# Kernel optimization log

Measured on AMD Instinct MI355X. Metric: run time of the kernel, lower is better.

The kernel has to match this reference:

```python
import jax, jax.numpy as jnp
import numpy as np

NUM_USERS = 100000
NUM_ITEMS = 50000
NUM_EDGES = 1000000
EMB_DIM = 64


def setup_inputs() -> dict:
    key = jax.random.key(0)
    k1, k2, k3, k4, k5, k6 = jax.random.split(key, 6)
    return {
        "user_emb": jax.random.normal(k1, (NUM_USERS, EMB_DIM), dtype=jnp.float32),
        "item_emb": jax.random.normal(k2, (NUM_ITEMS, EMB_DIM), dtype=jnp.float32),
        "u_sw": jax.random.uniform(k3, (NUM_USERS, 1), dtype=jnp.float32),
        "i_sw": jax.random.uniform(k4, (NUM_ITEMS, 1), dtype=jnp.float32),
        "edge_src_user": jax.random.randint(k5, (NUM_EDGES,), 0, NUM_USERS, dtype=jnp.int32),
        "edge_dst_item": jax.random.randint(k6, (NUM_EDGES,), 0, NUM_ITEMS, dtype=jnp.int32),
    }


def _segment_mean(feat_src, src_idx, dst_idx, num_dst, inv_deg):
    # gather source node features onto edges, sum-reduce at destinations, divide by degree
    s = jax.ops.segment_sum(feat_src[src_idx], dst_idx, num_segments=num_dst)
    return s * inv_deg


def reference(user_emb, item_emb, u_sw, i_sw, edge_src_user, edge_dst_item):
    ones = jnp.ones((edge_src_user.shape[0],), dtype=user_emb.dtype)
    deg_i = jax.ops.segment_sum(ones, edge_dst_item, num_segments=NUM_ITEMS)
    deg_u = jax.ops.segment_sum(ones, edge_src_user, num_segments=NUM_USERS)
    # DGL mean gives 0 for zero-degree nodes
    inv_deg_i = jnp.where(deg_i > 0, 1.0 / jnp.maximum(deg_i, 1.0), 0.0)[:, None]
    inv_deg_u = jnp.where(deg_u > 0, 1.0 / jnp.maximum(deg_u, 1.0), 0.0)[:, None]

    def one_round(u, i):
        # 'like': user -> item mean aggregation; 'rev_like': item -> user
        new_i = _segment_mean(u, edge_src_user, edge_dst_item, NUM_ITEMS, inv_deg_i)
        new_u = _segment_mean(i, edge_dst_item, edge_src_user, NUM_USERS, inv_deg_u)
        return new_u + u * u_sw, new_i + i * i_sw

    u, i = one_round(user_emb, item_emb)
    u, i = one_round(u, i)
    return (u, i)
```

## Files before the change

kernel.cpp:

```cpp
#include <hip/hip_runtime.h>
#include <hip/hip_fp16.h>

#define NU 100000
#define NI 50000
#define NE 1000000
#define D  64
#define NBI 196
#define NBU 391
#define NB_TOT (NBI + NBU)
#define CHUNK 2048
#define PART_K (CHUNK / 256)

__device__ __forceinline__ unsigned short f2h(float f) {
    return __half_as_ushort(__float2half(f));
}
__device__ __forceinline__ float h2f(unsigned short h) {
    return __half2float(__ushort_as_half(h));
}

__global__ void k_bhist_cvt(const int* __restrict__ esrc, const int* __restrict__ edst,
                            int* __restrict__ bcnt,
                            const float* __restrict__ ue, const float* __restrict__ ie,
                            unsigned short* __restrict__ u0h, unsigned short* __restrict__ i0h) {
    __shared__ int h[NB_TOT];
    for (int b = threadIdx.x; b < NB_TOT; b += blockDim.x) h[b] = 0;
    __syncthreads();
    int gt = blockIdx.x * blockDim.x + threadIdx.x;
    int gs = gridDim.x * blockDim.x;
    for (int e = gt; e < NE; e += gs) {
        atomicAdd(&h[edst[e] >> 8], 1);
        atomicAdd(&h[NBI + (esrc[e] >> 8)], 1);
    }
    const float4* uf = (const float4*)ue;
    ushort4* uh = (ushort4*)u0h;
    for (int i = gt; i < NU * (D / 4); i += gs) {
        float4 v = uf[i];
        ushort4 o; o.x = f2h(v.x); o.y = f2h(v.y); o.z = f2h(v.z); o.w = f2h(v.w);
        uh[i] = o;
    }
    const float4* if4 = (const float4*)ie;
    ushort4* ih = (ushort4*)i0h;
    for (int i = gt; i < NI * (D / 4); i += gs) {
        float4 v = if4[i];
        ushort4 o; o.x = f2h(v.x); o.y = f2h(v.y); o.z = f2h(v.z); o.w = f2h(v.w);
        ih[i] = o;
    }
    __syncthreads();
    for (int b = threadIdx.x; b < NB_TOT; b += blockDim.x) {
        int v = h[b];
        if (v) atomicAdd(&bcnt[b], v);
    }
}

__global__ void k_bscan_both(const int* __restrict__ bcnt,
                             int* __restrict__ bbase_i, int* __restrict__ gcur_i,
                             int* __restrict__ bbase_u, int* __restrict__ gcur_u) {
    __shared__ int s[512];
    int tid = threadIdx.x;
    const int* in = (blockIdx.x == 0) ? bcnt : bcnt + NBI;
    int nb        = (blockIdx.x == 0) ? NBI : NBU;
    int* bbase    = (blockIdx.x == 0) ? bbase_i : bbase_u;
    int* gcur     = (blockIdx.x == 0) ? gcur_i : gcur_u;
    int v = (tid < nb) ? in[tid] : 0;
    s[tid] = v;
    __syncthreads();
    for (int o = 1; o < 512; o <<= 1) {
        int t = (tid >= o) ? s[tid - o] : 0;
        __syncthreads();
        s[tid] += t;
        __syncthreads();
    }
    if (tid < nb) { int ex = s[tid] - v; bbase[tid] = ex; gcur[tid] = ex; }
    if (tid == 0) bbase[nb] = NE;
}

__global__ void k_part_both(const int* __restrict__ esrc, const int* __restrict__ edst,
                            int* __restrict__ gcur_i, int* __restrict__ gcur_u,
                            unsigned int* __restrict__ rec_i, unsigned int* __restrict__ rec_u) {
    __shared__ int cnt_i[NBI], gb_i[NBI], cnt_u[NBU], gb_u[NBU];
    int tid = threadIdx.x;
    for (int b = tid; b < NBI; b += 256) cnt_i[b] = 0;
    for (int b = tid; b < NBU; b += 256) cnt_u[b] = 0;
    __syncthreads();
    int base = blockIdx.x * CHUNK;
    int dd[PART_K], uu[PART_K], ki[PART_K], ku[PART_K];
#pragma unroll
    for (int k = 0; k < PART_K; k++) {
        int j = base + tid + k * 256;
        dd[k] = -1;
        if (j < NE) {
            dd[k] = edst[j]; uu[k] = esrc[j];
            ki[k] = atomicAdd(&cnt_i[dd[k] >> 8], 1);
            ku[k] = atomicAdd(&cnt_u[uu[k] >> 8], 1);
        }
    }
    __syncthreads();
    for (int b = tid; b < NBI; b += 256) { int v = cnt_i[b]; if (v) gb_i[b] = atomicAdd(&gcur_i[b], v); }
    for (int b = tid; b < NBU; b += 256) { int v = cnt_u[b]; if (v) gb_u[b] = atomicAdd(&gcur_u[b], v); }
    __syncthreads();
#pragma unroll
    for (int k = 0; k < PART_K; k++) {
        if (dd[k] >= 0) {
            rec_i[gb_i[dd[k] >> 8] + ki[k]] = ((unsigned int)(dd[k] & 255) << 17) | (unsigned int)uu[k];
            rec_u[gb_u[uu[k] >> 8] + ku[k]] = ((unsigned int)(uu[k] & 255) << 17) | (unsigned int)dd[k];
        }
    }
}

__global__ void k_local_both(const unsigned int* __restrict__ rec_i, const unsigned int* __restrict__ rec_u,
                             const int* __restrict__ bbase_i, const int* __restrict__ bbase_u,
                             int* __restrict__ rp_i, int* __restrict__ rp_u,
                             int* __restrict__ col_i, int* __restrict__ col_u) {
    __shared__ int cnt[256];
    __shared__ int off[256];
    int tid = threadIdx.x;
    int t = blockIdx.x;
    bool item = t < NBI;
    int b = item ? t : t - NBI;
    const unsigned int* rec = item ? rec_i : rec_u;
    const int* bb = item ? bbase_i : bbase_u;
    int* rp  = item ? rp_i : rp_u;
    int* col = item ? col_i : col_u;
    int nn   = item ? NI : NU;
    int beg = bb[b], end = bb[b + 1];
    cnt[tid] = 0;
    __syncthreads();
    for (int j = beg + tid; j < end; j += 256)
        atomicAdd(&cnt[rec[j] >> 17], 1);
    __syncthreads();
    int v = cnt[tid];
    off[tid] = v;
    __syncthreads();
    for (int o = 1; o < 256; o <<= 1) {
        int tv = (tid >= o) ? off[tid - o] : 0;
        __syncthreads();
        off[tid] += tv;
        __syncthreads();
    }
    int ex = off[tid] - v;
    int node = b * 256 + tid;
    if (node <= nn) rp[node] = beg + ex;
    cnt[tid] = ex;
    __syncthreads();
    for (int j = beg + tid; j < end; j += 256) {
        unsigned int r = rec[j];
        int p = atomicAdd(&cnt[r >> 17], 1);
        col[beg + p] = (int)(r & 0x1FFFF);
    }
}

template<bool WF, bool WH>
__device__ __forceinline__ void agg_h(const unsigned short* __restrict__ feat,
        const unsigned short* selfh, const float* __restrict__ sw,
        const int* __restrict__ rp, const int* __restrict__ cols,
        float* __restrict__ outf, unsigned short* outh,
        int n, int li, int lb) {
    int beg = rp[n], end = rp[n + 1];
    float swv = sw[n];
    ushort4 s4 = *(const ushort4*)(selfh + (size_t)n * D + li * 4);
    float ax = 0.f, ay = 0.f, az = 0.f, aw = 0.f;
    for (int j0 = beg; j0 < end; j0 += 16) {
        int cv = (j0 + li < end) ? cols[j0 + li] : 0;
        int nj = end - j0;
        ushort4 h[16];
#pragma unroll
        for (int j = 0; j < 16; j++) {
            int c = __shfl(cv, lb + j, 64);
            h[j] = *(const ushort4*)(feat + (size_t)c * D + li * 4);
        }
#pragma unroll
        for (int j = 0; j < 16; j++) {
            float w = (j < nj) ? 1.0f : 0.0f;
            ax = fmaf(w, h2f(h[j].x), ax);
            ay = fmaf(w, h2f(h[j].y), ay);
            az = fmaf(w, h2f(h[j].z), az);
            aw = fmaf(w, h2f(h[j].w), aw);
        }
    }
    int dgr = end - beg;
    float inv = (dgr > 0) ? (1.0f / (float)dgr) : 0.0f;
    float rx = ax * inv + h2f(s4.x) * swv;
    float ry = ay * inv + h2f(s4.y) * swv;
    float rz = az * inv + h2f(s4.z) * swv;
    float rw = aw * inv + h2f(s4.w) * swv;
    if (WH) {
        ushort4 o; o.x = f2h(rx); o.y = f2h(ry); o.z = f2h(rz); o.w = f2h(rw);
        *(ushort4*)(outh + (size_t)n * D + li * 4) = o;
    }
    if (WF) {
        float4 o; o.x = rx; o.y = ry; o.z = rz; o.w = rw;
        *(float4*)(outf + (size_t)n * D + li * 4) = o;
    }
}

__global__ __launch_bounds__(256) void k_agg_r1(
        const unsigned short* __restrict__ u0h, const unsigned short* __restrict__ i0h,
        const float* __restrict__ u_sw, const float* __restrict__ i_sw,
        const int* __restrict__ rp_i, const int* __restrict__ rp_u,
        const int* __restrict__ col_i, const int* __restrict__ col_u,
        unsigned short* __restrict__ i1h, unsigned short* __restrict__ u1h) {
    int g  = (blockIdx.x * blockDim.x + threadIdx.x) >> 4;
    int li = threadIdx.x & 15;
    int lb = threadIdx.x & 48;
    if (g < NI)
        agg_h<false, true>(u0h, i0h, i_sw, rp_i, col_i, nullptr, i1h, g, li, lb);
    else
        agg_h<false, true>(i0h, u0h, u_sw, rp_u, col_u, nullptr, u1h, g - NI, li, lb);
}

__global__ __launch_bounds__(256) void k_agg_r1i(
        const unsigned short* __restrict__ u0h, const unsigned short* __restrict__ i0h,
        const float* __restrict__ i_sw,
        const int* __restrict__ rp_i, const int* __restrict__ col_i,
        unsigned short* __restrict__ i1h) {
    int g  = (blockIdx.x * blockDim.x + threadIdx.x) >> 4;
    if (g >= NI) return;
    agg_h<false, true>(u0h, i0h, i_sw, rp_i, col_i, nullptr, i1h, g, threadIdx.x & 15, threadIdx.x & 48);
}
__global__ __launch_bounds__(256) void k_agg_r1u(
        const unsigned short* __restrict__ i0h, const unsigned short* u0h,
        const float* __restrict__ u_sw,
        const int* __restrict__ rp_u, const int* __restrict__ col_u,
        unsigned short* u1h) {
    int g  = (blockIdx.x * blockDim.x + threadIdx.x) >> 4;
    if (g >= NU) return;
    agg_h<false, true>(i0h, u0h, u_sw, rp_u, col_u, nullptr, u1h, g, threadIdx.x & 15, threadIdx.x & 48);
}

__global__ __launch_bounds__(256) void k_agg_r2(
        const unsigned short* __restrict__ u1h, const unsigned short* __restrict__ i1h,
        const float* __restrict__ u_sw, const float* __restrict__ i_sw,
        const int* __restrict__ rp_i, const int* __restrict__ rp_u,
        const int* __restrict__ col_i, const int* __restrict__ col_u,
        float* __restrict__ out_i, float* __restrict__ out_u) {
    int g  = (blockIdx.x * blockDim.x + threadIdx.x) >> 4;
    int li = threadIdx.x & 15;
    int lb = threadIdx.x & 48;
    if (g < NI)
        agg_h<true, false>(u1h, i1h, i_sw, rp_i, col_i, out_i, nullptr, g, li, lb);
    else
        agg_h<true, false>(i1h, u1h, u_sw, rp_u, col_u, out_u, nullptr, g - NI, li, lb);
}

extern "C" void kernel_launch(void* const* d_in, const int* in_sizes, int n_in,
                              void* d_out, int out_size, void* d_ws, size_t ws_size,
                              hipStream_t stream) {
    const float* user_emb = (const float*)d_in[0];
    const float* item_emb = (const float*)d_in[1];
    const float* u_sw     = (const float*)d_in[2];
    const float* i_sw     = (const float*)d_in[3];
    const int*   esrc     = (const int*)d_in[4];
    const int*   edst     = (const int*)d_in[5];

    float* out_u = (float*)d_out;
    float* out_i = out_u + NU * D;

    int* bcnt    = (int*)d_ws;
    int* bbase_i = bcnt + NB_TOT;
    int* bbase_u = bbase_i + NBI + 1;
    int* gcur_i  = bbase_u + NBU + 1;
    int* gcur_u  = gcur_i + NBI;
    int* rp_i    = gcur_u + NBU;
    int* rp_u    = rp_i + NI + 1;
    int* col_i   = rp_u + NU + 1;
    int* col_u   = col_i + NE;
    uintptr_t pa = ((uintptr_t)(col_u + NE) + 15) & ~(uintptr_t)15;
    unsigned short* u0h = (unsigned short*)pa;
    unsigned short* i0h = u0h + (size_t)NU * D;
    uintptr_t pc = (uintptr_t)(i0h + (size_t)NI * D);
    unsigned int* rec_i = (unsigned int*)pc;
    unsigned int* rec_u = rec_i + NE;
    unsigned short* i1h = (unsigned short*)pc;
    uintptr_t pd = (uintptr_t)(rec_u + NE);
    unsigned short* u1h_big = (unsigned short*)pd;
    size_t need = (pd + (size_t)NU * D * sizeof(unsigned short)) - (uintptr_t)d_ws;
    bool bigws = ws_size >= need;
    unsigned short* u1h = bigws ? u1h_big : u0h;

    hipMemsetAsync(bcnt, 0, NB_TOT * sizeof(int), stream);

    const int B = 256;

    k_bhist_cvt<<<1024, B, 0, stream>>>(esrc, edst, bcnt, user_emb, item_emb, u0h, i0h);
    k_bscan_both<<<2, 512, 0, stream>>>(bcnt, bbase_i, gcur_i, bbase_u, gcur_u);
    k_part_both<<<(NE + CHUNK - 1) / CHUNK, B, 0, stream>>>(esrc, edst, gcur_i, gcur_u, rec_i, rec_u);
    k_local_both<<<NB_TOT, B, 0, stream>>>(rec_i, rec_u, bbase_i, bbase_u, rp_i, rp_u, col_i, col_u);

    if (bigws) {
        k_agg_r1<<<((NI + NU) * 16) / B, B, 0, stream>>>(u0h, i0h, u_sw, i_sw,
                                                         rp_i, rp_u, col_i, col_u,
                                                         i1h, u1h);
    } else {
        k_agg_r1i<<<(NI * 16) / B, B, 0, stream>>>(u0h, i0h, i_sw, rp_i, col_i, i1h);
        k_agg_r1u<<<(NU * 16) / B, B, 0, stream>>>(i0h, u0h, u_sw, rp_u, col_u, u1h);
    }
    k_agg_r2<<<((NI + NU) * 16) / B, B, 0, stream>>>(u1h, i1h, u_sw, i_sw,
                                                     rp_i, rp_u, col_i, col_u,
                                                     out_i, out_u);
}
```

Before: 278.8 us.

## Fuse CSR build stages into one cooperative kernel with grid syncs

Replaces the memset plus four CSR-construction kernels (histogram/convert, scan, partition, local sort) with a single cooperative persistent kernel that uses grid.sync between phases. The aim is to remove per-launch overhead and inter-kernel gaps. The grid is capped at 512 blocks of 512 threads, and the old multi-kernel path is kept as a fallback. In exchange, the partition and local phases run on fewer blocks than before, and each grid-wide barrier has its own cost.

Measured after the change: 486.8 us. 74.6% more time.

```diff
diff --git a/kernel.cpp b/kernel.cpp
--- a/kernel.cpp
+++ b/kernel.cpp
@@ -1,5 +1,8 @@
 #include <hip/hip_runtime.h>
 #include <hip/hip_fp16.h>
+#include <hip/hip_cooperative_groups.h>
+
+namespace cg = cooperative_groups;
 
 #define NU 100000
 #define NI 50000
@@ -8,14 +11,162 @@
 #define NBI 196
 #define NBU 391
 #define NB_TOT (NBI + NBU)
+
 #define CHUNK 2048
 #define PART_K (CHUNK / 256)
 
+#define BT 512
+#define BCHUNK 4096
+#define BPART_K (BCHUNK / BT)
+
 __device__ __forceinline__ unsigned short f2h(float f) {
     return __half_as_ushort(__float2half(f));
 }
 __device__ __forceinline__ float h2f(unsigned short h) {
     return __half2float(__ushort_as_half(h));
+}
+
+__global__ __launch_bounds__(BT, 4) void k_build(
+        const int* __restrict__ esrc, const int* __restrict__ edst,
+        const float* __restrict__ ue, const float* __restrict__ ie,
+        unsigned short* __restrict__ u0h, unsigned short* __restrict__ i0h,
+        int* __restrict__ bcnt,
+        int* __restrict__ bbase_i, int* __restrict__ gcur_i,
+        int* __restrict__ bbase_u, int* __restrict__ gcur_u,
+        unsigned int* __restrict__ rec_i, unsigned int* __restrict__ rec_u,
+        int* __restrict__ rp_i, int* __restrict__ rp_u,
+        int* __restrict__ col_i, int* __restrict__ col_u)
+{
+    cg::grid_group grid = cg::this_grid();
+    const int tid = threadIdx.x;
+    const int gt = blockIdx.x * BT + tid;
+    const int gs = gridDim.x * BT;
+
+    __shared__ int h[NB_TOT];
+    __shared__ int s[BT];
+    __shared__ int cnt_i[NBI], gb_i[NBI];
+    __shared__ int cnt_u[NBU], gb_u[NBU];
+    __shared__ int lcnt[256], loff[256];
+
+    for (int b = tid; b < NB_TOT; b += BT) h[b] = 0;
+    for (int i = gt; i < NB_TOT; i += gs) bcnt[i] = 0;
+    __syncthreads();
+    for (int e = gt; e < NE; e += gs) {
+        atomicAdd(&h[edst[e] >> 8], 1);
+        atomicAdd(&h[NBI + (esrc[e] >> 8)], 1);
+    }
+    {
+        const float4* uf = (const float4*)ue;
+        ushort4* uh = (ushort4*)u0h;
+        for (int i = gt; i < NU * (D / 4); i += gs) {
+            float4 v = uf[i];
+            ushort4 o; o.x = f2h(v.x); o.y = f2h(v.y); o.z = f2h(v.z); o.w = f2h(v.w);
+            uh[i] = o;
+        }
+        const float4* if4 = (const float4*)ie;
+        ushort4* ih = (ushort4*)i0h;
+        for (int i = gt; i < NI * (D / 4); i += gs) {
+            float4 v = if4[i];
+            ushort4 o; o.x = f2h(v.x); o.y = f2h(v.y); o.z = f2h(v.z); o.w = f2h(v.w);
+            ih[i] = o;
+        }
+    }
+    grid.sync();
+
+    for (int b = tid; b < NB_TOT; b += BT) {
+        int v = h[b];
+        if (v) atomicAdd(&bcnt[b], v);
+    }
+    grid.sync();
+
+    if (blockIdx.x < 2) {
+        const int* in = (blockIdx.x == 0) ? bcnt : bcnt + NBI;
+        int nb2       = (blockIdx.x == 0) ? NBI : NBU;
+        int* bbase    = (blockIdx.x == 0) ? bbase_i : bbase_u;
+        int* gcur     = (blockIdx.x == 0) ? gcur_i : gcur_u;
+        int v = (tid < nb2) ? in[tid] : 0;
+        s[tid] = v;
+        __syncthreads();
+        for (int o = 1; o < BT; o <<= 1) {
+            int t = (tid >= o) ? s[tid - o] : 0;
+            __syncthreads();
+            s[tid] += t;
+            __syncthreads();
+        }
+        if (tid < nb2) { int ex = s[tid] - v; bbase[tid] = ex; gcur[tid] = ex; }
+        if (tid == 0) bbase[nb2] = NE;
+    }
+    grid.sync();
+
+    const int nchunk = (NE + BCHUNK - 1) / BCHUNK;
+    for (int c = blockIdx.x; c < nchunk; c += gridDim.x) {
+        for (int b = tid; b < NBI; b += BT) cnt_i[b] = 0;
+        for (int b = tid; b < NBU; b += BT) cnt_u[b] = 0;
+        __syncthreads();
+        int base = c * BCHUNK;
+        int dd[BPART_K], uu[BPART_K], ki[BPART_K], ku[BPART_K];
+#pragma unroll
+        for (int k = 0; k < BPART_K; k++) {
+            int j = base + tid + k * BT;
+            dd[k] = -1;
+            if (j < NE) {
+                dd[k] = edst[j]; uu[k] = esrc[j];
+                ki[k] = atomicAdd(&cnt_i[dd[k] >> 8], 1);
+                ku[k] = atomicAdd(&cnt_u[uu[k] >> 8], 1);
+            }
+        }
+        __syncthreads();
+        for (int b = tid; b < NBI; b += BT) { int v = cnt_i[b]; if (v) gb_i[b] = atomicAdd(&gcur_i[b], v); }
+        for (int b = tid; b < NBU; b += BT) { int v = cnt_u[b]; if (v) gb_u[b] = atomicAdd(&gcur_u[b], v); }
+        __syncthreads();
+#pragma unroll
+        for (int k = 0; k < BPART_K; k++) {
+            if (dd[k] >= 0) {
+                rec_i[gb_i[dd[k] >> 8] + ki[k]] = ((unsigned int)(dd[k] & 255) << 17) | (unsigned int)uu[k];
+                rec_u[gb_u[uu[k] >> 8] + ku[k]] = ((unsigned int)(uu[k] & 255) << 17) | (unsigned int)dd[k];
+            }
+        }
+        __syncthreads();
+    }
+    grid.sync();
+
+    for (int t = blockIdx.x; t < NB_TOT; t += gridDim.x) {
+        bool item = t < NBI;
+        int b = item ? t : t - NBI;
+        const unsigned int* rec = item ? rec_i : rec_u;
+        const int* bb = item ? bbase_i : bbase_u;
+        int* rp  = item ? rp_i : rp_u;
+        int* col = item ? col_i : col_u;
+        int nn   = item ? NI : NU;
+        int beg = bb[b], end = bb[b + 1];
+        if (tid < 256) lcnt[tid] = 0;
+        __syncthreads();
+        for (int j = beg + tid; j < end; j += BT)
+            atomicAdd(&lcnt[rec[j] >> 17], 1);
+        __syncthreads();
+        int v = (tid < 256) ? lcnt[tid] : 0;
+        if (tid < 256) loff[tid] = v;
+        __syncthreads();
+        for (int o = 1; o < 256; o <<= 1) {
+            int tv = (tid >= o && tid < 256) ? loff[tid - o] : 0;
+            __syncthreads();
+            if (tid < 256) loff[tid] += tv;
+            __syncthreads();
+        }
+        if (tid < 256) {
+            int ex = loff[tid] - v;
+            int node = b * 256 + tid;
+            if (node <= nn) rp[node] = beg + ex;
+            lcnt[tid] = ex;
+        }
+        __syncthreads();
+        for (int j = beg + tid; j < end; j += BT) {
+            unsigned int r = rec[j];
+            int p = atomicAdd(&lcnt[r >> 17], 1);
+            col[beg + p] = (int)(r & 0x1FFFF);
+        }
+        __syncthreads();
+    }
 }
 
 __global__ void k_bhist_cvt(const int* __restrict__ esrc, const int* __restrict__ edst,
@@ -277,14 +428,43 @@
     bool bigws = ws_size >= need;
     unsigned short* u1h = bigws ? u1h_big : u0h;
 
-    hipMemsetAsync(bcnt, 0, NB_TOT * sizeof(int), stream);
-
     const int B = 256;
 
-    k_bhist_cvt<<<1024, B, 0, stream>>>(esrc, edst, bcnt, user_emb, item_emb, u0h, i0h);
-    k_bscan_both<<<2, 512, 0, stream>>>(bcnt, bbase_i, gcur_i, bbase_u, gcur_u);
-    k_part_both<<<(NE + CHUNK - 1) / CHUNK, B, 0, stream>>>(esrc, edst, gcur_i, gcur_u, rec_i, rec_u);
-    k_local_both<<<NB_TOT, B, 0, stream>>>(rec_i, rec_u, bbase_i, bbase_u, rp_i, rp_u, col_i, col_u);
+    static int coopG = -2;
+    if (coopG == -2) {
+        int nb = 0;
+        hipError_t e = hipOccupancyMaxActiveBlocksPerMultiprocessor(
+            &nb, reinterpret_cast<const void*>(k_build), BT, 0);
+        int cus = 0;
+        hipError_t e2 = hipDeviceGetAttribute(&cus, hipDeviceAttributeMultiprocessorCount, 0);
+        if (e == hipSuccess && e2 == hipSuccess && nb > 0 && cus > 0) {
+            long cap = (long)nb * cus;
+            coopG = (int)(cap > 512 ? 512 : cap);
+            if (coopG < 2) coopG = 0;
+        } else {
+            coopG = 0;
+        }
+    }
+
+    bool coop_done = false;
+    if (coopG > 0) {
+        void* args[] = { (void*)&esrc, (void*)&edst, (void*)&user_emb, (void*)&item_emb,
+                         (void*)&u0h, (void*)&i0h, (void*)&bcnt,
+                         (void*)&bbase_i, (void*)&gcur_i, (void*)&bbase_u, (void*)&gcur_u,
+                         (void*)&rec_i, (void*)&rec_u, (void*)&rp_i, (void*)&rp_u,
+                         (void*)&col_i, (void*)&col_u };
+        hipError_t err = hipLaunchCooperativeKernel(
+            reinterpret_cast<const void*>(k_build), dim3(coopG), dim3(BT), args, 0, stream);
+        if (err == hipSuccess) coop_done = true;
+        else coopG = 0;
+    }
+    if (!coop_done) {
+        hipMemsetAsync(bcnt, 0, NB_TOT * sizeof(int), stream);
+        k_bhist_cvt<<<1024, B, 0, stream>>>(esrc, edst, bcnt, user_emb, item_emb, u0h, i0h);
+        k_bscan_both<<<2, 512, 0, stream>>>(bcnt, bbase_i, gcur_i, bbase_u, gcur_u);
+        k_part_both<<<(NE + CHUNK - 1) / CHUNK, B, 0, stream>>>(esrc, edst, gcur_i, gcur_u, rec_i, rec_u);
+        k_local_both<<<NB_TOT, B, 0, stream>>>(rec_i, rec_u, bbase_i, bbase_u, rp_i, rp_u, col_i, col_u);
+    }
 
     if (bigws) {
         k_agg_r1<<<((NI + NU) * 16) / B, B, 0, stream>>>(u0h, i0h, u_sw, i_sw,
```
